# Optimization experiments

Hardware: AMD Instinct MI355X
Metric: run time of the kernel (lower is better)

Reference implementation:

```python
import jax, jax.numpy as jnp
import numpy as np
from jax import lax

N = 2048
P = 256
F_J = 0.05      # sparsity of recurrent matrix J
F_OUT = 0.05    # sparsity of readout
DT = 0.1
ON_TIME = 10
T = 200


def _activation(x):
    # Tanh_shifted_and_scaled: rates in [0, 1]
    return 0.5 * (1.0 + jnp.tanh(x))


def setup_inputs() -> dict:
    key = jax.random.key(0)
    k1, k2, k3, k4, k5 = jax.random.split(key, 5)
    # patterns ~ Uniform(-1, 1), shape [N, P]
    patterns = jax.random.uniform(k1, (N, P), jnp.float32, -1.0, 1.0)
    # sparse recurrent matrix J: gaussian values, density F_J, gain g
    g = 10.0 * 0.1 ** 0.25 / np.sqrt(N * P * np.sqrt(F_J))
    J_dense = jax.random.normal(k2, (N, N), jnp.float32) * jnp.float32(g)
    mask = jax.random.uniform(k3, (N, N)) < F_J
    J = jnp.where(mask, J_dense, 0.0).astype(jnp.float32)
    # sparse readout: ones at a random F_OUT fraction of units (frozen)
    w_out = (jax.random.uniform(k4, (N,)) < F_OUT).astype(jnp.float32)
    return {"patterns": patterns, "J": J, "w_out": w_out, "N_time_steps": T}


def reference(patterns, J, w_out, N_time_steps):
    # Batched over all P patterns at once (columns of [N, P] state).
    n = patterns.shape[0]
    x0 = jnp.zeros_like(patterns)           # [N, P]
    r0 = _activation(x0)

    def step(carry, ti):
        x, rates = carry
        inp = jnp.where(ti < ON_TIME, patterns, 0.0)      # [N, P]
        x = x + DT * (-x + J @ rates + inp)               # [N, P]
        rates = _activation(x)
        out_t = w_out @ rates                             # [P]
        return (x, rates), out_t

    _, outs = lax.scan(step, (x0, r0), jnp.arange(N_time_steps))  # [T, P]
    readout = outs.T / n                                   # [P, T]
    return readout
```

## Files before the change

kernel.cpp:

```cpp
#include <hip/hip_runtime.h>
#include <hip/hip_bf16.h>


#define NN 2048
#define PP 256
#define DT_C 0.1f
#define ON_TIME_C 10

typedef __attribute__((ext_vector_type(8)))  short bf16x8;
typedef __attribute__((ext_vector_type(16))) float f32x16;

__device__ __forceinline__ unsigned short bf16rne(float f) {
    unsigned b = __float_as_uint(f);
    return (unsigned short)((b + 0x7FFFu + ((b >> 16) & 1u)) >> 16);
}
__device__ __forceinline__ int kperm16(int s) {
    return (s & 3) + (((s >> 2) & 1) << 3) + ((s >> 3) << 2);
}

__global__ void convert_J_kernel(const float* __restrict__ J,
                                 unsigned short* __restrict__ Jp) {
    int i = blockIdx.x * blockDim.x + threadIdx.x;
    int row = i >> 11, k = i & 2047;
    Jp[((size_t)row << 11) + (k & ~15) + kperm16(k & 15)] = bf16rne(J[i]);
}

__global__ void init_kernel(float* __restrict__ x,
                            unsigned short* __restrict__ rT,
                            float* __restrict__ out, int nout) {
    int i = blockIdx.x * blockDim.x + threadIdx.x;
    x[i] = 0.0f;
    rT[i] = 0x3F00;
    if (i < nout) out[i] = 0.0f;
}

#define AS1 __attribute__((address_space(1)))
#define AS3 __attribute__((address_space(3)))
#define GLOAD16(g, l) \
    __builtin_amdgcn_global_load_lds((const AS1 void*)(g), (AS3 void*)(l), 16, 0, 0)

__global__ __launch_bounds__(1024, 1) void gemm_step_kernel(
    const unsigned short* __restrict__ Jp,
    const unsigned short* __restrict__ rin,
    unsigned short* __restrict__ rout,
    float* __restrict__ x, const float* __restrict__ patterns,
    const float* __restrict__ w_out, float* __restrict__ out,
    int t, int T, int with_input) {

    __shared__ char smem[98304];

    const int tid  = threadIdx.x;
    const int wv   = tid >> 6;
    const int lane = tid & 63;
    const int s    = wv >> 3;
    const int kq   = wv & 7;
    const int h    = lane >> 5;

    const int bid   = (blockIdx.x & 7) * 32 + (blockIdx.x >> 3);
    const int mbase = (bid >> 3) * 64;
    const int nbase = (bid & 7) * 32;

    const int p   = tid & 31;
    const int ra0 = tid >> 5;
    const int ra1 = 32 + ra0;
    const char* gA0 = (const char*)Jp  + (((size_t)(mbase + ra0)) << 12)
                      + ((p ^ (ra0 & 15)) << 4);
    const char* gA1 = (const char*)Jp  + (((size_t)(mbase + ra1)) << 12)
                      + ((p ^ (ra1 & 15)) << 4);
    const char* gB  = (const char*)rin + (((size_t)(nbase + ra0)) << 12)
                      + ((p ^ (ra0 & 15)) << 4);
    const int ldsA0 = 1024 * wv;
    const int ldsA1 = 16384 + 1024 * wv;
    const int ldsB  = 32768 + 1024 * wv;

    const int rA  = 32 * s + (lane & 31);
    const int rBn = lane & 31;

    f32x16 acc = {};

    GLOAD16(gA0, smem + ldsA0);
    GLOAD16(gA1, smem + ldsA1);
    GLOAD16(gB,  smem + ldsB);

    #pragma unroll
    for (int ph = 0; ph < 8; ++ph) {
        asm volatile("s_waitcnt vmcnt(0)" ::: "memory");
        __builtin_amdgcn_s_barrier();
        if (ph < 7) {
            const int bo = ((ph + 1) & 1) * 49152;
            GLOAD16(gA0 + (ph + 1) * 512, smem + bo + ldsA0);
            GLOAD16(gA1 + (ph + 1) * 512, smem + bo + ldsA1);
            GLOAD16(gB  + (ph + 1) * 512, smem + bo + ldsB);
        }
        __builtin_amdgcn_sched_barrier(0);

        const int bb = (ph & 1) * 49152;
        #pragma unroll
        for (int sl = 0; sl < 2; ++sl) {
            const int c = (kq * 2 + sl) * 2 + h;
            bf16x8 a = *(const bf16x8*)(smem + bb + rA * 512
                                        + ((c ^ (rA & 15)) << 4));
            bf16x8 b = *(const bf16x8*)(smem + bb + 32768 + rBn * 512
                                        + ((c ^ (rBn & 15)) << 4));
            acc = __builtin_amdgcn_mfma_f32_32x32x16_bf16(a, b, acc, 0, 0, 0);
        }
    }

    __syncthreads();

    {
        float* pf = (float*)smem;
        const int plane = (s * 8 + kq) * 1024;
        #pragma unroll
        for (int reg = 0; reg < 16; ++reg) {
            int row = (reg & 3) + 8 * (reg >> 2) + 4 * h;
            pf[plane + row * 32 + (lane & 31)] = acc[reg];
        }
    }
    __syncthreads();

    {
        const int mloc = tid >> 4;
        const int c2   = (tid & 15) * 2;
        const int s2   = mloc >> 5;
        const float* pf = (const float*)smem;
        float2 sum = make_float2(0.f, 0.f);
        #pragma unroll
        for (int q = 0; q < 8; ++q) {
            float2 v = *(const float2*)(pf + (s2 * 8 + q) * 1024
                                        + (mloc & 31) * 32 + c2);
            sum.x += v.x; sum.y += v.y;
        }

        const int m  = mbase + mloc;
        const int n0 = nbase + c2;
        size_t xo = ((size_t)m << 8) + n0;
        float2 xv = *(const float2*)(x + xo);
        float2 pv = make_float2(0.f, 0.f);
        if (with_input) pv = *(const float2*)(patterns + xo);
        float wsc = (w_out[m] != 0.0f) ? (1.0f / (float)NN) : 0.0f;

        float xn0 = xv.x + DT_C * (sum.x + pv.x - xv.x);
        float xn1 = xv.y + DT_C * (sum.y + pv.y - xv.y);
        *(float2*)(x + xo) = make_float2(xn0, xn1);
        float r0f = 0.5f * (1.0f + tanhf(xn0));
        float r1f = 0.5f * (1.0f + tanhf(xn1));
        if (wsc != 0.0f) {
            atomicAdd(&out[(size_t)n0 * T + t],       r0f * wsc);
            atomicAdd(&out[(size_t)(n0 + 1) * T + t], r1f * wsc);
        }
        const int pos = (mloc & ~15) + kperm16(mloc & 15);
        int b0 = 65536 + c2 * 128       + (((pos >> 3) ^ (c2 & 7)) << 4)       + (pos & 7) * 2;
        int b1 = 65536 + (c2 + 1) * 128 + (((pos >> 3) ^ ((c2 + 1) & 7)) << 4) + (pos & 7) * 2;
        *(unsigned short*)(smem + b0) = bf16rne(r0f);
        *(unsigned short*)(smem + b1) = bf16rne(r1f);
    }
    __syncthreads();
    if (tid < 256) {
        int nl = tid >> 3, pc = tid & 7;
        uint4 v = *(const uint4*)(smem + 65536 + nl * 128 + ((pc ^ (nl & 7)) << 4));
        *(uint4*)((char*)rout + (((size_t)(nbase + nl)) << 12) + mbase * 2 + pc * 16) = v;
    }
}

extern "C" void kernel_launch(void* const* d_in, const int* in_sizes, int n_in,
                              void* d_out, int out_size, void* d_ws, size_t ws_size,
                              hipStream_t stream) {
    const float* patterns = (const float*)d_in[0];
    const float* J        = (const float*)d_in[1];
    const float* w_out    = (const float*)d_in[2];
    float* out            = (float*)d_out;

    int T = out_size / PP;

    size_t off = 0;
    auto alloc = [&](size_t bytes) {
        void* p = (char*)d_ws + off;
        off += (bytes + 255) & ~(size_t)255;
        return p;
    };
    unsigned short* Jp = (unsigned short*)alloc((size_t)NN * NN * 2);
    unsigned short* r0 = (unsigned short*)alloc((size_t)PP * NN * 2);
    unsigned short* r1 = (unsigned short*)alloc((size_t)PP * NN * 2);
    float*          x  = (float*)         alloc((size_t)NN * PP * 4);
    (void)ws_size; (void)n_in; (void)in_sizes;

    convert_J_kernel<<<(NN * NN) / 256, 256, 0, stream>>>(J, Jp);
    init_kernel<<<(NN * PP) / 256, 256, 0, stream>>>(x, r0, out, PP * T);

    for (int t = 0; t < T; ++t) {
        const unsigned short* rin = (t & 1) ? r1 : r0;
        unsigned short*      rout = (t & 1) ? r0 : r1;
        gemm_step_kernel<<<256, 1024, 0, stream>>>(Jp, rin, rout, x, patterns,
                                                   w_out, out, t, T,
                                                   (t < ON_TIME_C) ? 1 : 0);
    }
}
```

Baseline: 2.265 ms.

## Deepen K-loop pipeline to four smaller LDS stages with prefetch distance two

```diff
diff --git a/kernel.cpp b/kernel.cpp
--- a/kernel.cpp
+++ b/kernel.cpp
@@ -60,50 +60,53 @@
     const int mbase = (bid >> 3) * 64;
     const int nbase = (bid & 7) * 32;
 
-    const int p   = tid & 31;
-    const int ra0 = tid >> 5;
-    const int ra1 = 32 + ra0;
-    const char* gA0 = (const char*)Jp  + (((size_t)(mbase + ra0)) << 12)
-                      + ((p ^ (ra0 & 15)) << 4);
-    const char* gA1 = (const char*)Jp  + (((size_t)(mbase + ra1)) << 12)
-                      + ((p ^ (ra1 & 15)) << 4);
-    const char* gB  = (const char*)rin + (((size_t)(nbase + ra0)) << 12)
-                      + ((p ^ (ra0 & 15)) << 4);
-    const int ldsA0 = 1024 * wv;
-    const int ldsA1 = 16384 + 1024 * wv;
-    const int ldsB  = 32768 + 1024 * wv;
+    const int sr = tid >> 4;
+    const int sp = tid & 15;
+    const char* gA = (const char*)Jp + (((size_t)(mbase + sr)) << 12)
+                     + ((sp ^ (sr & 15)) << 4);
+    const int  ldsA = 1024 * wv;
+    const bool hasB = (wv >= 8);
+    const int  rb   = sr - 32;
+    const char* gB = (const char*)rin + (((size_t)(nbase + (hasB ? rb : 0))) << 12)
+                     + ((sp ^ (rb & 15)) << 4);
+    const int  ldsB = 16384 + 1024 * (wv - 8);
 
     const int rA  = 32 * s + (lane & 31);
     const int rBn = lane & 31;
 
     f32x16 acc = {};
 
-    GLOAD16(gA0, smem + ldsA0);
-    GLOAD16(gA1, smem + ldsA1);
-    GLOAD16(gB,  smem + ldsB);
+    GLOAD16(gA,       smem + 0 * 24576 + ldsA);
+    if (hasB) GLOAD16(gB,       smem + 0 * 24576 + ldsB);
+    GLOAD16(gA + 256, smem + 1 * 24576 + ldsA);
+    if (hasB) GLOAD16(gB + 256, smem + 1 * 24576 + ldsB);
 
     #pragma unroll
-    for (int ph = 0; ph < 8; ++ph) {
-        asm volatile("s_waitcnt vmcnt(0)" ::: "memory");
+    for (int ph = 0; ph < 16; ++ph) {
+        if (ph < 14) {
+            const int bo = ((ph + 2) & 3) * 24576;
+            GLOAD16(gA + (ph + 2) * 256, smem + bo + ldsA);
+            if (hasB) GLOAD16(gB + (ph + 2) * 256, smem + bo + ldsB);
+        }
+        if (wv < 8) {
+            if (ph < 14)       asm volatile("s_waitcnt vmcnt(2)" ::: "memory");
+            else if (ph == 14) asm volatile("s_waitcnt vmcnt(1)" ::: "memory");
+            else               asm volatile("s_waitcnt vmcnt(0)" ::: "memory");
+        } else {
+            if (ph < 14)       asm volatile("s_waitcnt vmcnt(4)" ::: "memory");
+            else if (ph == 14) asm volatile("s_waitcnt vmcnt(2)" ::: "memory");
+            else               asm volatile("s_waitcnt vmcnt(0)" ::: "memory");
+        }
         __builtin_amdgcn_s_barrier();
-        if (ph < 7) {
-            const int bo = ((ph + 1) & 1) * 49152;
-            GLOAD16(gA0 + (ph + 1) * 512, smem + bo + ldsA0);
-            GLOAD16(gA1 + (ph + 1) * 512, smem + bo + ldsA1);
-            GLOAD16(gB  + (ph + 1) * 512, smem + bo + ldsB);
-        }
         __builtin_amdgcn_sched_barrier(0);
 
-        const int bb = (ph & 1) * 49152;
-        #pragma unroll
-        for (int sl = 0; sl < 2; ++sl) {
-            const int c = (kq * 2 + sl) * 2 + h;
-            bf16x8 a = *(const bf16x8*)(smem + bb + rA * 512
-                                        + ((c ^ (rA & 15)) << 4));
-            bf16x8 b = *(const bf16x8*)(smem + bb + 32768 + rBn * 512
-                                        + ((c ^ (rBn & 15)) << 4));
-            acc = __builtin_amdgcn_mfma_f32_32x32x16_bf16(a, b, acc, 0, 0, 0);
-        }
+        const int bb = (ph & 3) * 24576;
+        const int c  = kq * 2 + h;
+        bf16x8 a = *(const bf16x8*)(smem + bb + rA * 256
+                                    + ((c ^ (rA & 15)) << 4));
+        bf16x8 b = *(const bf16x8*)(smem + bb + 16384 + rBn * 256
+                                    + ((c ^ (rBn & 15)) << 4));
+        acc = __builtin_amdgcn_mfma_f32_32x32x16_bf16(a, b, acc, 0, 0, 0);
     }
 
     __syncthreads();
```

After: 1.982 ms. -12.5%, faster.
